# Kernel tuning notes

Hardware: AMD Instinct MI355X
Metric: run time of the kernel (lower is better)

The kernel has to match this reference:

```python
import jax, jax.numpy as jnp
import numpy as np
import math

B, T, E, H = 2, 2048, 1024, 16
HD = E // H


def layernorm(x, g, b, eps=1e-5):
    mu = jnp.mean(x, axis=-1, keepdims=True)
    var = jnp.var(x, axis=-1, keepdims=True)
    return (x - mu) * jax.lax.rsqrt(var + eps) * g + b


def new_gelu(x):
    c = math.sqrt(2.0 / math.pi)
    return 0.5 * x * (1.0 + jnp.tanh(c * (x + 0.044715 * x ** 3)))


def setup_inputs() -> dict:
    key = jax.random.key(0)
    ks = jax.random.split(key, 6)
    s = 0.02
    return {
        "x": jax.random.normal(ks[0], (B, T, E), jnp.float32),
        "ln1_g": jnp.ones((E,), jnp.float32),
        "ln1_b": jnp.zeros((E,), jnp.float32),
        "w_attn": jax.random.normal(ks[1], (E, 3 * E), jnp.float32) * s,
        "b_attn": jnp.zeros((3 * E,), jnp.float32),
        "w_proj": jax.random.normal(ks[2], (E, E), jnp.float32) * s,
        "b_proj": jnp.zeros((E,), jnp.float32),
        "ln2_g": jnp.ones((E,), jnp.float32),
        "ln2_b": jnp.zeros((E,), jnp.float32),
        "w_fc": jax.random.normal(ks[3], (E, 4 * E), jnp.float32) * s,
        "b_fc": jnp.zeros((4 * E,), jnp.float32),
        "w_fc2": jax.random.normal(ks[4], (4 * E, E), jnp.float32) * s,
        "b_fc2": jnp.zeros((E,), jnp.float32),
    }


def reference(x, ln1_g, ln1_b, w_attn, b_attn, w_proj, b_proj,
              ln2_g, ln2_b, w_fc, b_fc, w_fc2, b_fc2):
    # --- attention branch (pre-norm) ---
    h = layernorm(x, ln1_g, ln1_b)
    qkv = h @ w_attn + b_attn                      # [B,T,3E]
    q, k, v = jnp.split(qkv, 3, axis=-1)
    # [B,T,E] -> [B,H,T,HD]
    q = q.reshape(B, T, H, HD).transpose(0, 2, 1, 3)
    k = k.reshape(B, T, H, HD).transpose(0, 2, 1, 3)
    v = v.reshape(B, T, H, HD).transpose(0, 2, 1, 3)
    att = jnp.einsum('bhqd,bhkd->bhqk', q, k) * (1.0 / math.sqrt(HD))
    causal = jnp.tril(jnp.ones((T, T), bool))       # [T,T]
    att = jnp.where(causal, att, -jnp.inf)
    att = jax.nn.softmax(att, axis=-1)
    y = jnp.einsum('bhqk,bhkd->bhqd', att, v)       # [B,H,T,HD]
    y = y.transpose(0, 2, 1, 3).reshape(B, T, E)
    y = y @ w_proj + b_proj
    x = x + y
    # --- MLP branch (pre-norm) ---
    h = layernorm(x, ln2_g, ln2_b)
    h = new_gelu(h @ w_fc + b_fc)
    h = h @ w_fc2 + b_fc2
    return x + h
```

## Files before the change

### kernel.cpp

```cpp
#include <hip/hip_runtime.h>

typedef unsigned short u16;
typedef unsigned int   u32;
typedef short bf16x8 __attribute__((ext_vector_type(8)));
typedef float f32x4  __attribute__((ext_vector_type(4)));

__device__ __forceinline__ float bf_lo(u32 u){ return __uint_as_float(u << 16); }
__device__ __forceinline__ float bf_hi(u32 u){ return __uint_as_float(u & 0xffff0000u); }
__device__ __forceinline__ u16 bf16r(float f){
  u32 u = __float_as_uint(f);
  u += 0x7fffu + ((u >> 16) & 1u);
  return (u16)(u >> 16);
}
__device__ __forceinline__ u32 pack2(float a, float b){
  return (u32)bf16r(a) | ((u32)bf16r(b) << 16);
}
__device__ __forceinline__ u32 pk_trunc(float a, float b){
  return (__float_as_uint(a) >> 16) | (__float_as_uint(b) & 0xffff0000u);
}
__device__ __forceinline__ float gelu_f(float x){
  float t = 0.7978845608028654f * (x + 0.044715f * x * x * x);
  t = fminf(fmaxf(t, -12.f), 12.f);
  float e = __expf(2.f * t);
  float th = (e - 1.f) / (e + 1.f);
  return 0.5f * x * (1.f + th);
}
__device__ __forceinline__ void glds16(const void* g, void* l) {
  __builtin_amdgcn_global_load_lds(
      (const __attribute__((address_space(1))) void*)g,
      (__attribute__((address_space(3))) void*)l, 16, 0, 0);
}

#define QSCALE 0.1803368801111204f

__global__ __launch_bounds__(256) void wt_k(const float* __restrict__ W,
                                            u16* __restrict__ Wt, int K, int N) {
  __shared__ float t[32][33];
  int k0 = blockIdx.x * 32, n0 = blockIdx.y * 32;
  int tx = threadIdx.x & 31, ty = threadIdx.x >> 5;
  #pragma unroll
  for (int i = 0; i < 32; i += 8)
    t[ty + i][tx] = W[(size_t)(k0 + ty + i) * N + n0 + tx];
  __syncthreads();
  #pragma unroll
  for (int i = 0; i < 32; i += 8)
    Wt[(size_t)(n0 + ty + i) * K + k0 + tx] = bf16r(t[tx][ty + i]);
}

__global__ __launch_bounds__(256) void vt_k(const u16* __restrict__ qkv,
                                            u16* __restrict__ Vt) {
  __shared__ u16 tl[32][33];
  int t0 = blockIdx.x * 32;
  int bh = blockIdx.y >> 1, d0 = (blockIdx.y & 1) * 32;
  int bb = bh >> 4, h = bh & 15;
  int tx = threadIdx.x & 31, ty = threadIdx.x >> 5;
  #pragma unroll
  for (int i = 0; i < 32; i += 8)
    tl[ty + i][tx] = qkv[(size_t)(bb*2048 + t0 + ty + i)*3072 + 2048 + h*64 + d0 + tx];
  __syncthreads();
  #pragma unroll
  for (int i = 0; i < 32; i += 8)
    Vt[((size_t)bh*64 + d0 + ty + i)*2048 + t0 + tx] = tl[tx][ty + i];
}

__global__ __launch_bounds__(256) void ln_k(const float* __restrict__ x,
                                            const float* __restrict__ g,
                                            const float* __restrict__ bta,
                                            u16* __restrict__ out) {
  int row = blockIdx.x, tid = threadIdx.x;
  const float4 xv = ((const float4*)(x + (size_t)row * 1024))[tid];
  float s = xv.x + xv.y + xv.z + xv.w;
  float q = xv.x*xv.x + xv.y*xv.y + xv.z*xv.z + xv.w*xv.w;
  #pragma unroll
  for (int off = 32; off > 0; off >>= 1) {
    s += __shfl_down(s, off);
    q += __shfl_down(q, off);
  }
  __shared__ float ss[4], sq[4];
  if ((tid & 63) == 0) { ss[tid >> 6] = s; sq[tid >> 6] = q; }
  __syncthreads();
  s = ss[0] + ss[1] + ss[2] + ss[3];
  q = sq[0] + sq[1] + sq[2] + sq[3];
  float mu = s * (1.f/1024.f);
  float rs = rsqrtf(q * (1.f/1024.f) - mu*mu + 1e-5f);
  const float4 gv = ((const float4*)g)[tid];
  const float4 bv = ((const float4*)bta)[tid];
  uint2 o;
  o.x = pack2((xv.x-mu)*rs*gv.x + bv.x, (xv.y-mu)*rs*gv.y + bv.y);
  o.y = pack2((xv.z-mu)*rs*gv.z + bv.z, (xv.w-mu)*rs*gv.w + bv.w);
  ((uint2*)(out + (size_t)row * 1024))[tid] = o;
}

template<int MODE, int MI, int LB>
__global__ __launch_bounds__(256, LB) void gemm_k(
    const u16* __restrict__ A, const u16* __restrict__ Bt,
    const float* __restrict__ bias, const float* __restrict__ resid,
    void* __restrict__ out, int M, int N, int K, int lda)
{
  constexpr int TM = MI * 32;
  __shared__ u16 Al[TM * 64];
  __shared__ u16 Bl[128 * 64];
  const int tid = threadIdx.x;
  const int by = blockIdx.y;
  const int sp = (MODE == 5) ? (by >> 3) : 0;
  const int n0 = (MODE == 5) ? ((by & 7) * 128) : (by * 128);
  const size_t koff = (size_t)sp * K;
  const int m0 = blockIdx.x * TM;
  const int wave = tid >> 6, lane = tid & 63;
  const int wm = (wave >> 1) * (MI * 16), wn = (wave & 1) * 64;
  const int l15 = lane & 15, quad = lane >> 4;
  const int sr = lane >> 3, cs = lane & 7;
  f32x4 acc[MI][4];
  const f32x4 zero = {0.f, 0.f, 0.f, 0.f};
  #pragma unroll
  for (int i = 0; i < MI; ++i)
    #pragma unroll
    for (int j = 0; j < 4; ++j)
      acc[i][j] = zero;
  for (int k0 = 0; k0 < K; k0 += 64) {
    __syncthreads();
    #pragma unroll
    for (int it = 0; it < MI; ++it) {
      int r = it*32 + wave*8 + sr;
      int c = cs ^ (r & 7);
      glds16(&A[(size_t)(m0 + r) * lda + koff + k0 + c*8], &Al[(it*32 + wave*8) * 64]);
    }
    #pragma unroll
    for (int it = 0; it < 4; ++it) {
      int r = it*32 + wave*8 + sr;
      int c = cs ^ (r & 7);
      glds16(&Bt[(size_t)(n0 + r) * lda + koff + k0 + c*8], &Bl[(it*32 + wave*8) * 64]);
    }
    __syncthreads();
    #pragma unroll
    for (int kk = 0; kk < 2; ++kk) {
      bf16x8 af[MI], bfr[4];
      #pragma unroll
      for (int i = 0; i < MI; ++i) {
        int R = wm + i*16 + l15;
        af[i] = *(const bf16x8*)&Al[R*64 + ((kk*4 + quad) ^ (R & 7)) * 8];
      }
      #pragma unroll
      for (int j = 0; j < 4; ++j) {
        int R = wn + j*16 + l15;
        bfr[j] = *(const bf16x8*)&Bl[R*64 + ((kk*4 + quad) ^ (R & 7)) * 8];
      }
      #pragma unroll
      for (int i = 0; i < MI; ++i)
        #pragma unroll
        for (int j = 0; j < 4; ++j)
          acc[i][j] = __builtin_amdgcn_mfma_f32_16x16x32_bf16(af[i], bfr[j], acc[i][j], 0, 0, 0);
    }
  }
  #pragma unroll
  for (int i = 0; i < MI; ++i) {
    #pragma unroll
    for (int j = 0; j < 4; ++j) {
      int col = n0 + wn + j*16 + l15;
      float bv = (MODE == 5) ? 0.f : bias[col];
      float sc = (MODE == 4 && col < 1024) ? QSCALE : 1.0f;
      #pragma unroll
      for (int r = 0; r < 4; ++r) {
        int row = m0 + wm + i*16 + quad*4 + r;
        size_t idx = (size_t)row * N + col;
        float v = acc[i][j][r] + bv;
        if constexpr (MODE == 0)      ((u16*)out)[idx] = bf16r(v);
        else if constexpr (MODE == 1) ((float*)out)[idx] = v + resid[idx];
        else if constexpr (MODE == 2) ((u16*)out)[idx] = bf16r(gelu_f(v));
        else if constexpr (MODE == 4) ((u16*)out)[idx] = bf16r(v * sc);
        else if constexpr (MODE == 5) ((u16*)out)[(size_t)sp*M*N + idx] = bf16r(v);
        else                          ((float*)out)[idx] = v + resid[idx];
      }
    }
  }
}

__global__ __launch_bounds__(256) void cmb_k(const u16* __restrict__ p,
                                             const float* __restrict__ bias,
                                             const float* __restrict__ x2,
                                             float* __restrict__ out) {
  int row = blockIdx.x, t = threadIdx.x;
  size_t i = (size_t)row * 1024 + t*4;
  uint2 a = *(const uint2*)&p[i];
  uint2 b = *(const uint2*)&p[4194304 + i];
  float4 xv = ((const float4*)x2)[i >> 2];
  float4 bv = ((const float4*)bias)[t];
  float4 o;
  o.x = bf_lo(a.x) + bf_lo(b.x) + bv.x + xv.x;
  o.y = bf_hi(a.x) + bf_hi(b.x) + bv.y + xv.y;
  o.z = bf_lo(a.y) + bf_lo(b.y) + bv.z + xv.z;
  o.w = bf_hi(a.y) + bf_hi(b.y) + bv.w + xv.w;
  ((float4*)out)[i >> 2] = o;
}

__global__ __launch_bounds__(256, 2) void attn_k(const u16* __restrict__ qkv,
                                                 const u16* __restrict__ Vt,
                                                 u16* __restrict__ y) {
  __shared__ u16 Kl[2][64*64];
  __shared__ u16 Vl[2][64*64];
  __shared__ u16 Pw[4*16*72];
  const int tid = threadIdx.x;
  const int bh = blockIdx.x & 31, bb = bh >> 4, h = bh & 15;
  const int tt = blockIdx.x >> 5;
  const int qt = (tt < 8) ? tt : 23 - tt;
  const int w = tid >> 6, lane = tid & 63;
  const int l15 = lane & 15, quad = lane >> 4;
  const int sr = lane >> 3, cs = lane & 7;
  u16* Pme = Pw + w * (16*72);
  const int w16l = w*16 + l15;
  const int dquad = quad*4;

  bf16x8 aq[2][2];
  #pragma unroll
  for (int g = 0; g < 2; ++g) {
    const u16* qp = qkv + ((size_t)(bb*2048 + qt*128 + g*64 + w16l))*3072
                    + h*64 + quad*8;
    aq[g][0] = *(const bf16x8*)qp;
    aq[g][1] = *(const bf16x8*)(qp + 32);
  }
  f32x4 o[2][4];
  const f32x4 zero = {0.f,0.f,0.f,0.f};
  #pragma unroll
  for (int g = 0; g < 2; ++g)
    #pragma unroll
    for (int dt = 0; dt < 4; ++dt) o[g][dt] = zero;
  float l[2] = {0.f, 0.f};
  const int last = 2*qt + 1;

  const u16* kbase = qkv + (size_t)bb*2048*3072 + 1024 + h*64;
  const u16* vbase = Vt + (size_t)bh*64*2048;

  #pragma unroll
  for (int it = 0; it < 2; ++it) {
    int r = it*32 + w*8 + sr;
    int c = cs ^ (r & 7);
    glds16(kbase + (size_t)r*3072 + c*8, &Kl[0][(it*32 + w*8) * 64]);
    glds16(vbase + (size_t)r*2048 + c*8, &Vl[0][(it*32 + w*8) * 64]);
  }

  int p = 0;
  for (int kt = 0; kt <= last; ++kt) {
    __syncthreads();
    if (kt < last) {
      #pragma unroll
      for (int it = 0; it < 2; ++it) {
        int r = it*32 + w*8 + sr;
        int c = cs ^ (r & 7);
        glds16(kbase + (size_t)((kt+1)*64 + r)*3072 + c*8, &Kl[p^1][(it*32 + w*8) * 64]);
        glds16(vbase + (size_t)r*2048 + (kt+1)*64 + c*8,   &Vl[p^1][(it*32 + w*8) * 64]);
      }
    }
    bf16x8 ak[4][2], av[4][2];
    #pragma unroll
    for (int nt = 0; nt < 4; ++nt) {
      int R = nt*16 + l15;
      #pragma unroll
      for (int kk = 0; kk < 2; ++kk) {
        ak[nt][kk] = *(const bf16x8*)&Kl[p][R*64 + ((kk*4 + quad) ^ (R & 7)) * 8];
        av[nt][kk] = *(const bf16x8*)&Vl[p][R*64 + ((kk*4 + quad) ^ (R & 7)) * 8];
      }
    }
    #pragma unroll
    for (int g = 0; g < 2; ++g) {
      if (kt > 2*qt + g) continue;
      f32x4 sv[4];
      #pragma unroll
      for (int nt = 0; nt < 4; ++nt) {
        f32x4 s = zero;
        s = __builtin_amdgcn_mfma_f32_16x16x32_bf16(ak[nt][0], aq[g][0], s, 0, 0, 0);
        s = __builtin_amdgcn_mfma_f32_16x16x32_bf16(ak[nt][1], aq[g][1], s, 0, 0, 0);
        sv[nt] = s;
      }
      if (kt == 2*qt + g) {
        #pragma unroll
        for (int nt = 0; nt < 4; ++nt)
          #pragma unroll
          for (int r = 0; r < 4; ++r)
            if (nt*16 + dquad + r > w16l) sv[nt][r] = -1e30f;
      }
      float pv[4][4];
      #pragma unroll
      for (int nt = 0; nt < 4; ++nt)
        #pragma unroll
        for (int r = 0; r < 4; ++r)
          pv[nt][r] = exp2f(sv[nt][r]);
      l[g] += ((pv[0][0]+pv[0][1])+(pv[0][2]+pv[0][3]))
            + ((pv[1][0]+pv[1][1])+(pv[1][2]+pv[1][3]))
            + ((pv[2][0]+pv[2][1])+(pv[2][2]+pv[2][3]))
            + ((pv[3][0]+pv[3][1])+(pv[3][2]+pv[3][3]));
      #pragma unroll
      for (int nt = 0; nt < 4; ++nt) {
        uint2 pr;
        pr.x = pk_trunc(pv[nt][0], pv[nt][1]);
        pr.y = pk_trunc(pv[nt][2], pv[nt][3]);
        *(uint2*)&Pme[l15*72 + nt*16 + dquad] = pr;
      }
      const bf16x8 bp0 = *(const bf16x8*)&Pme[l15*72 + quad*8];
      const bf16x8 bp1 = *(const bf16x8*)&Pme[l15*72 + 32 + quad*8];
      #pragma unroll
      for (int dt = 0; dt < 4; ++dt) {
        o[g][dt] = __builtin_amdgcn_mfma_f32_16x16x32_bf16(av[dt][0], bp0, o[g][dt], 0, 0, 0);
        o[g][dt] = __builtin_amdgcn_mfma_f32_16x16x32_bf16(av[dt][1], bp1, o[g][dt], 0, 0, 0);
      }
    }
    p ^= 1;
  }
  #pragma unroll
  for (int g = 0; g < 2; ++g) {
    float lt = l[g];
    lt += __shfl_xor(lt, 16);
    lt += __shfl_xor(lt, 32);
    float inv = 1.f / lt;
    u16* yp = y + ((size_t)(bb*2048 + qt*128 + g*64 + w16l))*1024 + h*64;
    #pragma unroll
    for (int dt = 0; dt < 4; ++dt) {
      uint2 pk;
      pk.x = pack2(o[g][dt][0]*inv, o[g][dt][1]*inv);
      pk.y = pack2(o[g][dt][2]*inv, o[g][dt][3]*inv);
      *(uint2*)(yp + dt*16 + dquad) = pk;
    }
  }
}

extern "C" void kernel_launch(void* const* d_in, const int* in_sizes, int n_in,
                              void* d_out, int out_size, void* d_ws, size_t ws_size,
                              hipStream_t stream) {
  const float* x      = (const float*)d_in[0];
  const float* ln1_g  = (const float*)d_in[1];
  const float* ln1_b  = (const float*)d_in[2];
  const float* w_attn = (const float*)d_in[3];
  const float* b_attn = (const float*)d_in[4];
  const float* w_proj = (const float*)d_in[5];
  const float* b_proj = (const float*)d_in[6];
  const float* ln2_g  = (const float*)d_in[7];
  const float* ln2_b  = (const float*)d_in[8];
  const float* w_fc   = (const float*)d_in[9];
  const float* b_fc   = (const float*)d_in[10];
  const float* w_fc2  = (const float*)d_in[11];
  const float* b_fc2  = (const float*)d_in[12];

  char* ws = (char*)d_ws;
  u16*   wt_attn = (u16*)(ws);
  u16*   wt_proj = (u16*)(ws + 6291456);
  u16*   wt_fc   = (u16*)(ws + 8388608);
  u16*   wt_fc2  = (u16*)(ws + 16777216);
  u16*   h1      = (u16*)(ws + 25165824);
  u16*   qkvb    = (u16*)(ws + 33554432);
  u16*   yb      = (u16*)(ws + 58720256);
  float* x2      = (float*)(ws + 67108864);
  u16*   h2  = h1;
  u16*   vtb = h1;
  u16*   act = qkvb;
  u16*   pk2 = (u16*)(ws);

  wt_k<<<dim3(32, 96),  256, 0, stream>>>(w_attn, wt_attn, 1024, 3072);
  wt_k<<<dim3(32, 32),  256, 0, stream>>>(w_proj, wt_proj, 1024, 1024);
  wt_k<<<dim3(32, 128), 256, 0, stream>>>(w_fc,   wt_fc,   1024, 4096);
  wt_k<<<dim3(128, 32), 256, 0, stream>>>(w_fc2,  wt_fc2,  4096, 1024);

  ln_k<<<4096, 256, 0, stream>>>(x, ln1_g, ln1_b, h1);
  gemm_k<4,4,3><<<dim3(32, 24), 256, 0, stream>>>(h1, wt_attn, b_attn, nullptr,
                                                  (void*)qkvb, 4096, 3072, 1024, 1024);
  vt_k<<<dim3(64, 64), 256, 0, stream>>>(qkvb, vtb);
  attn_k<<<dim3(512), 256, 0, stream>>>(qkvb, vtb, yb);
  gemm_k<1,2,4><<<dim3(64, 8), 256, 0, stream>>>(yb, wt_proj, b_proj, x,
                                                 (void*)x2, 4096, 1024, 1024, 1024);
  ln_k<<<4096, 256, 0, stream>>>(x2, ln2_g, ln2_b, h2);
  gemm_k<2,4,3><<<dim3(32, 32), 256, 0, stream>>>(h2, wt_fc, b_fc, nullptr,
                                                  (void*)act, 4096, 4096, 1024, 1024);
  gemm_k<5,2,4><<<dim3(64, 16), 256, 0, stream>>>(act, wt_fc2, b_fc2, nullptr,
                                                  (void*)pk2, 4096, 1024, 2048, 4096);
  cmb_k<<<4096, 256, 0, stream>>>(pk2, b_fc2, x2, (float*)d_out);
}
```

Before: 344.7 us.

## Shrink attention query tile, single-buffer K/V, raise occupancy; retune GEMM tiles

The attention kernel now handles one 64-row query tile per block instead of two, launches twice as many blocks and allows four blocks per CU. K/V staging is single-buffered with a barrier before and after each load, and query tiles are scheduled longest-first. This aims to improve parallelism and occupancy, but it gives up load/compute overlap and doubles K/V traffic per query row. Several GEMM launches also change their template tile parameters and grid sizes.

```diff
diff --git a/kernel.cpp b/kernel.cpp
--- a/kernel.cpp
+++ b/kernel.cpp
@@ -193,16 +193,15 @@
   ((float4*)out)[i >> 2] = o;
 }
 
-__global__ __launch_bounds__(256, 2) void attn_k(const u16* __restrict__ qkv,
+__global__ __launch_bounds__(256, 4) void attn_k(const u16* __restrict__ qkv,
                                                  const u16* __restrict__ Vt,
                                                  u16* __restrict__ y) {
-  __shared__ u16 Kl[2][64*64];
-  __shared__ u16 Vl[2][64*64];
+  __shared__ u16 Kl[64*64];
+  __shared__ u16 Vl[64*64];
   __shared__ u16 Pw[4*16*72];
   const int tid = threadIdx.x;
   const int bh = blockIdx.x & 31, bb = bh >> 4, h = bh & 15;
-  const int tt = blockIdx.x >> 5;
-  const int qt = (tt < 8) ? tt : 23 - tt;
+  const int qt = 31 - (int)(blockIdx.x >> 5);
   const int w = tid >> 6, lane = tid & 63;
   const int l15 = lane & 15, quad = lane >> 4;
   const int sr = lane >> 3, cs = lane & 7;
@@ -210,115 +209,90 @@
   const int w16l = w*16 + l15;
   const int dquad = quad*4;
 
-  bf16x8 aq[2][2];
-  #pragma unroll
-  for (int g = 0; g < 2; ++g) {
-    const u16* qp = qkv + ((size_t)(bb*2048 + qt*128 + g*64 + w16l))*3072
-                    + h*64 + quad*8;
-    aq[g][0] = *(const bf16x8*)qp;
-    aq[g][1] = *(const bf16x8*)(qp + 32);
-  }
-  f32x4 o[2][4];
+  const u16* qp = qkv + ((size_t)(bb*2048 + qt*64 + w16l))*3072 + h*64 + quad*8;
+  const bf16x8 aq0 = *(const bf16x8*)qp;
+  const bf16x8 aq1 = *(const bf16x8*)(qp + 32);
+
+  f32x4 o[4];
   const f32x4 zero = {0.f,0.f,0.f,0.f};
   #pragma unroll
-  for (int g = 0; g < 2; ++g)
-    #pragma unroll
-    for (int dt = 0; dt < 4; ++dt) o[g][dt] = zero;
-  float l[2] = {0.f, 0.f};
-  const int last = 2*qt + 1;
+  for (int dt = 0; dt < 4; ++dt) o[dt] = zero;
+  float l = 0.f;
 
   const u16* kbase = qkv + (size_t)bb*2048*3072 + 1024 + h*64;
   const u16* vbase = Vt + (size_t)bh*64*2048;
 
-  #pragma unroll
-  for (int it = 0; it < 2; ++it) {
-    int r = it*32 + w*8 + sr;
-    int c = cs ^ (r & 7);
-    glds16(kbase + (size_t)r*3072 + c*8, &Kl[0][(it*32 + w*8) * 64]);
-    glds16(vbase + (size_t)r*2048 + c*8, &Vl[0][(it*32 + w*8) * 64]);
-  }
-
-  int p = 0;
-  for (int kt = 0; kt <= last; ++kt) {
+  for (int kt = 0; kt <= qt; ++kt) {
     __syncthreads();
-    if (kt < last) {
-      #pragma unroll
-      for (int it = 0; it < 2; ++it) {
-        int r = it*32 + w*8 + sr;
-        int c = cs ^ (r & 7);
-        glds16(kbase + (size_t)((kt+1)*64 + r)*3072 + c*8, &Kl[p^1][(it*32 + w*8) * 64]);
-        glds16(vbase + (size_t)r*2048 + (kt+1)*64 + c*8,   &Vl[p^1][(it*32 + w*8) * 64]);
-      }
-    }
+    #pragma unroll
+    for (int it = 0; it < 2; ++it) {
+      int r = it*32 + w*8 + sr;
+      int c = cs ^ (r & 7);
+      glds16(kbase + (size_t)(kt*64 + r)*3072 + c*8, &Kl[(it*32 + w*8) * 64]);
+      glds16(vbase + (size_t)r*2048 + kt*64 + c*8,   &Vl[(it*32 + w*8) * 64]);
+    }
+    __syncthreads();
     bf16x8 ak[4][2], av[4][2];
     #pragma unroll
     for (int nt = 0; nt < 4; ++nt) {
       int R = nt*16 + l15;
       #pragma unroll
       for (int kk = 0; kk < 2; ++kk) {
-        ak[nt][kk] = *(const bf16x8*)&Kl[p][R*64 + ((kk*4 + quad) ^ (R & 7)) * 8];
-        av[nt][kk] = *(const bf16x8*)&Vl[p][R*64 + ((kk*4 + quad) ^ (R & 7)) * 8];
+        ak[nt][kk] = *(const bf16x8*)&Kl[R*64 + ((kk*4 + quad) ^ (R & 7)) * 8];
+        av[nt][kk] = *(const bf16x8*)&Vl[R*64 + ((kk*4 + quad) ^ (R & 7)) * 8];
       }
     }
-    #pragma unroll
-    for (int g = 0; g < 2; ++g) {
-      if (kt > 2*qt + g) continue;
-      f32x4 sv[4];
-      #pragma unroll
-      for (int nt = 0; nt < 4; ++nt) {
-        f32x4 s = zero;
-        s = __builtin_amdgcn_mfma_f32_16x16x32_bf16(ak[nt][0], aq[g][0], s, 0, 0, 0);
-        s = __builtin_amdgcn_mfma_f32_16x16x32_bf16(ak[nt][1], aq[g][1], s, 0, 0, 0);
-        sv[nt] = s;
-      }
-      if (kt == 2*qt + g) {
-        #pragma unroll
-        for (int nt = 0; nt < 4; ++nt)
-          #pragma unroll
-          for (int r = 0; r < 4; ++r)
-            if (nt*16 + dquad + r > w16l) sv[nt][r] = -1e30f;
-      }
-      float pv[4][4];
+    f32x4 sv[4];
+    #pragma unroll
+    for (int nt = 0; nt < 4; ++nt) {
+      f32x4 s = zero;
+      s = __builtin_amdgcn_mfma_f32_16x16x32_bf16(ak[nt][0], aq0, s, 0, 0, 0);
+      s = __builtin_amdgcn_mfma_f32_16x16x32_bf16(ak[nt][1], aq1, s, 0, 0, 0);
+      sv[nt] = s;
+    }
+    if (kt == qt) {
       #pragma unroll
       for (int nt = 0; nt < 4; ++nt)
         #pragma unroll
         for (int r = 0; r < 4; ++r)
-          pv[nt][r] = exp2f(sv[nt][r]);
-      l[g] += ((pv[0][0]+pv[0][1])+(pv[0][2]+pv[0][3]))
-            + ((pv[1][0]+pv[1][1])+(pv[1][2]+pv[1][3]))
-            + ((pv[2][0]+pv[2][1])+(pv[2][2]+pv[2][3]))
-            + ((pv[3][0]+pv[3][1])+(pv[3][2]+pv[3][3]));
-      #pragma unroll
-      for (int nt = 0; nt < 4; ++nt) {
-        uint2 pr;
-        pr.x = pk_trunc(pv[nt][0], pv[nt][1]);
-        pr.y = pk_trunc(pv[nt][2], pv[nt][3]);
-        *(uint2*)&Pme[l15*72 + nt*16 + dquad] = pr;
-      }
-      const bf16x8 bp0 = *(const bf16x8*)&Pme[l15*72 + quad*8];
-      const bf16x8 bp1 = *(const bf16x8*)&Pme[l15*72 + 32 + quad*8];
-      #pragma unroll
-      for (int dt = 0; dt < 4; ++dt) {
-        o[g][dt] = __builtin_amdgcn_mfma_f32_16x16x32_bf16(av[dt][0], bp0, o[g][dt], 0, 0, 0);
-        o[g][dt] = __builtin_amdgcn_mfma_f32_16x16x32_bf16(av[dt][1], bp1, o[g][dt], 0, 0, 0);
-      }
-    }
-    p ^= 1;
-  }
-  #pragma unroll
-  for (int g = 0; g < 2; ++g) {
-    float lt = l[g];
-    lt += __shfl_xor(lt, 16);
-    lt += __shfl_xor(lt, 32);
-    float inv = 1.f / lt;
-    u16* yp = y + ((size_t)(bb*2048 + qt*128 + g*64 + w16l))*1024 + h*64;
+          if (nt*16 + dquad + r > w16l) sv[nt][r] = -1e30f;
+    }
+    float pv[4][4];
+    #pragma unroll
+    for (int nt = 0; nt < 4; ++nt)
+      #pragma unroll
+      for (int r = 0; r < 4; ++r)
+        pv[nt][r] = exp2f(sv[nt][r]);
+    l += ((pv[0][0]+pv[0][1])+(pv[0][2]+pv[0][3]))
+       + ((pv[1][0]+pv[1][1])+(pv[1][2]+pv[1][3]))
+       + ((pv[2][0]+pv[2][1])+(pv[2][2]+pv[2][3]))
+       + ((pv[3][0]+pv[3][1])+(pv[3][2]+pv[3][3]));
+    #pragma unroll
+    for (int nt = 0; nt < 4; ++nt) {
+      uint2 pr;
+      pr.x = pk_trunc(pv[nt][0], pv[nt][1]);
+      pr.y = pk_trunc(pv[nt][2], pv[nt][3]);
+      *(uint2*)&Pme[l15*72 + nt*16 + dquad] = pr;
+    }
+    const bf16x8 bp0 = *(const bf16x8*)&Pme[l15*72 + quad*8];
+    const bf16x8 bp1 = *(const bf16x8*)&Pme[l15*72 + 32 + quad*8];
     #pragma unroll
     for (int dt = 0; dt < 4; ++dt) {
-      uint2 pk;
-      pk.x = pack2(o[g][dt][0]*inv, o[g][dt][1]*inv);
-      pk.y = pack2(o[g][dt][2]*inv, o[g][dt][3]*inv);
-      *(uint2*)(yp + dt*16 + dquad) = pk;
-    }
+      o[dt] = __builtin_amdgcn_mfma_f32_16x16x32_bf16(av[dt][0], bp0, o[dt], 0, 0, 0);
+      o[dt] = __builtin_amdgcn_mfma_f32_16x16x32_bf16(av[dt][1], bp1, o[dt], 0, 0, 0);
+    }
+  }
+  float lt = l;
+  lt += __shfl_xor(lt, 16);
+  lt += __shfl_xor(lt, 32);
+  float inv = 1.f / lt;
+  u16* yp = y + ((size_t)(bb*2048 + qt*64 + w16l))*1024 + h*64;
+  #pragma unroll
+  for (int dt = 0; dt < 4; ++dt) {
+    uint2 pk;
+    pk.x = pack2(o[dt][0]*inv, o[dt][1]*inv);
+    pk.y = pack2(o[dt][2]*inv, o[dt][3]*inv);
+    *(uint2*)(yp + dt*16 + dquad) = pk;
   }
 }
 
@@ -359,16 +333,16 @@
   wt_k<<<dim3(128, 32), 256, 0, stream>>>(w_fc2,  wt_fc2,  4096, 1024);
 
   ln_k<<<4096, 256, 0, stream>>>(x, ln1_g, ln1_b, h1);
-  gemm_k<4,4,3><<<dim3(32, 24), 256, 0, stream>>>(h1, wt_attn, b_attn, nullptr,
+  gemm_k<4,2,3><<<dim3(64, 24), 256, 0, stream>>>(h1, wt_attn, b_attn, nullptr,
                                                   (void*)qkvb, 4096, 3072, 1024, 1024);
   vt_k<<<dim3(64, 64), 256, 0, stream>>>(qkvb, vtb);
-  attn_k<<<dim3(512), 256, 0, stream>>>(qkvb, vtb, yb);
-  gemm_k<1,2,4><<<dim3(64, 8), 256, 0, stream>>>(yb, wt_proj, b_proj, x,
+  attn_k<<<dim3(1024), 256, 0, stream>>>(qkvb, vtb, yb);
+  gemm_k<1,2,3><<<dim3(64, 8), 256, 0, stream>>>(yb, wt_proj, b_proj, x,
                                                  (void*)x2, 4096, 1024, 1024, 1024);
   ln_k<<<4096, 256, 0, stream>>>(x2, ln2_g, ln2_b, h2);
-  gemm_k<2,4,3><<<dim3(32, 32), 256, 0, stream>>>(h2, wt_fc, b_fc, nullptr,
+  gemm_k<2,2,3><<<dim3(64, 32), 256, 0, stream>>>(h2, wt_fc, b_fc, nullptr,
                                                   (void*)act, 4096, 4096, 1024, 1024);
-  gemm_k<5,2,4><<<dim3(64, 16), 256, 0, stream>>>(act, wt_fc2, b_fc2, nullptr,
+  gemm_k<5,2,3><<<dim3(64, 16), 256, 0, stream>>>(act, wt_fc2, b_fc2, nullptr,
                                                   (void*)pk2, 4096, 1024, 2048, 4096);
   cmb_k<<<4096, 256, 0, stream>>>(pk2, b_fc2, x2, (float*)d_out);
 }
```

New measurement: 346.9 us. Within noise of the previous version (+0.7%).
